# Performance work log

Measured on AMD Instinct MI355X. Metric: run time of the kernel, lower is better.

Reference implementation:

```python
import jax, jax.numpy as jnp
import numpy as np

B, NMAX, D, H = 8, 8192, 256, 8
DH = D // H  # 32
EPS = 1e-5


def _ln(x, g, b):
    mu = jnp.mean(x, axis=-1, keepdims=True)
    var = jnp.mean((x - mu) ** 2, axis=-1, keepdims=True)
    return (x - mu) / jnp.sqrt(var + EPS) * g + b


def setup_inputs() -> dict:
    key = jax.random.key(0)
    ks = jax.random.split(key, 14)
    s = 1.0 / np.sqrt(D)

    def lin(k):
        kw, kb = jax.random.split(k)
        W = jax.random.uniform(kw, (D, D), minval=-s, maxval=s, dtype=jnp.float32)
        b = jax.random.uniform(kb, (D,), minval=-s, maxval=s, dtype=jnp.float32)
        return W, b

    Wh, bh = lin(ks[0])
    Wq, bq = lin(ks[1])
    Wk, bk = lin(ks[2])
    Wv, bv = lin(ks[3])
    Wout, bout = lin(ks[4])
    return {
        "x": jax.random.normal(ks[5], (B * NMAX, D), dtype=jnp.float32),
        "node_prob": jax.random.uniform(ks[6], (B, NMAX), dtype=jnp.float32),
        "Wh": Wh, "bh": bh,
        "Wq": Wq, "bq": bq,
        "Wk": Wk, "bk": bk,
        "Wv": Wv, "bv": bv,
        "Wout": Wout, "bout": bout,
        "ln1_g": jnp.ones((D,), jnp.float32), "ln1_b": jnp.zeros((D,), jnp.float32),
        "ln2_g": jnp.ones((D,), jnp.float32), "ln2_b": jnp.zeros((D,), jnp.float32),
        "beta_b": jnp.full((D,), 0.5, jnp.float32),  # self.b with beta=0.5 >= 0
    }


def reference(x, node_prob, Wh, bh, Wq, bq, Wk, bk, Wv, bv, Wout, bout,
              ln1_g, ln1_b, ln2_g, ln2_b, beta_b):
    x0 = _ln(x, ln1_g, ln1_b)          # [N, D] input_norm
    h = x0 @ Wh + bh                   # [N, D]
    xd = x0.reshape(B, NMAX, D)        # to_dense_batch (equal-size graphs)
    k = jax.nn.sigmoid(xd @ Wk + bk)   # [B, Nmax, D]
    q = jax.nn.sigmoid(xd @ Wq + bq)   # qk_shared=False
    v = xd @ Wv + bv
    k = k * node_prob[:, :, None]      # node-prob weighting
    q = q.reshape(B, NMAX, H, DH)
    k = k.reshape(B, NMAX, H, DH)
    v = v.reshape(B, NMAX, H, DH)
    kv = jnp.einsum('bnhd,bnhe->bhde', k, v)        # k^T v per head
    num = jnp.einsum('bnhd,bhde->bnhe', q, kv)      # q . kv
    den = jnp.einsum('bnhd,bhd->bnh', q, jnp.sum(k, axis=1))[..., None]
    att = (num / den).reshape(B * NMAX, D)
    out = _ln(att, ln2_g, ln2_b) * (h + beta_b)     # norm(x) * (h + beta)
    out = jax.nn.relu(out @ Wout + bout)            # dropout p=0 / eval: identity
    return out + x0                                  # residual=True
```

## Files before the change

kernel.cpp:

```cpp
#include <hip/hip_runtime.h>
#include <cstdint>


#define DEVI __device__ __forceinline__

typedef __attribute__((ext_vector_type(8))) short bf16x8;
typedef __attribute__((ext_vector_type(4))) float f32x4;

DEVI ushort f2bf(float f) {
  uint32_t u = __float_as_uint(f);
  u += 0x7FFFu + ((u >> 16) & 1u);
  return (ushort)(u >> 16);
}
DEVI float bf2f(ushort h) { return __uint_as_float(((uint32_t)h) << 16); }

DEVI void gload_lds16(const void* g, void* l) {
  __builtin_amdgcn_global_load_lds((const __attribute__((address_space(1))) void*)g,
                                   (__attribute__((address_space(3))) void*)l, 16, 0, 0);
}
DEVI void vm_drain() { asm volatile("s_waitcnt vmcnt(0)" ::: "memory"); }

__global__ __launch_bounds__(256)
void prep_k(const float* __restrict__ Wh, const float* __restrict__ Wq,
            const float* __restrict__ Wk, const float* __restrict__ Wv,
            const float* __restrict__ Wout,
            const float* __restrict__ bh, const float* __restrict__ bq,
            const float* __restrict__ bk, const float* __restrict__ bv,
            ushort* __restrict__ Wcat_t, ushort* __restrict__ Woutt,
            float* __restrict__ bcat, float* __restrict__ kv, float* __restrict__ ksum)
{
  int idx = blockIdx.x * 256 + threadIdx.x;
  if (idx < 262144) {
    int j = idx >> 8, kk = idx & 255;
    int g = j >> 8, jj = j & 255;
    const float* W = (g == 0) ? Wh : (g == 1) ? Wq : (g == 2) ? Wk : Wv;
    Wcat_t[idx] = f2bf(W[kk * 256 + jj]);
  }
  int i2 = idx - 262144;
  if (i2 >= 0 && i2 < 65536) {
    int j = i2 >> 8, kk = i2 & 255;
    Woutt[i2] = f2bf(Wout[kk * 256 + j]);
  }
  int i3 = idx - (262144 + 65536);
  if (i3 >= 0 && i3 < 1024) {
    int g = i3 >> 8, jj = i3 & 255;
    const float* bb = (g == 0) ? bh : (g == 1) ? bq : (g == 2) ? bk : bv;
    bcat[i3] = bb[jj];
  }
  int i4 = idx - (262144 + 65536 + 1024);
  if (i4 >= 0 && i4 < 65536) kv[i4] = 0.0f;
  int i5 = idx - (262144 + 65536 + 1024 + 65536);
  if (i5 >= 0 && i5 < 2048) ksum[i5] = 0.0f;
}

__global__ __launch_bounds__(256)
void ln1_k(const float* __restrict__ x, const float* __restrict__ g1,
           const float* __restrict__ b1, ushort* __restrict__ x0b)
{
  const int t = threadIdx.x, l = t & 63, w = t >> 6;
  const size_t r = (size_t)blockIdx.x * 4 + w;
  const float4 xv = *(const float4*)&x[r * 256 + l * 4];
  float s = xv.x + xv.y + xv.z + xv.w;
  float sq = xv.x * xv.x + xv.y * xv.y + xv.z * xv.z + xv.w * xv.w;
#pragma unroll
  for (int off = 1; off < 64; off <<= 1) { s += __shfl_xor(s, off); sq += __shfl_xor(sq, off); }
  const float mean = s * (1.0f / 256.0f);
  const float var = sq * (1.0f / 256.0f) - mean * mean;
  const float rstd = rsqrtf(var + 1e-5f);
  const float4 g4 = *(const float4*)&g1[l * 4];
  const float4 b4 = *(const float4*)&b1[l * 4];
  ushort4 o;
  o.x = f2bf((xv.x - mean) * rstd * g4.x + b4.x);
  o.y = f2bf((xv.y - mean) * rstd * g4.y + b4.y);
  o.z = f2bf((xv.z - mean) * rstd * g4.z + b4.z);
  o.w = f2bf((xv.w - mean) * rstd * g4.w + b4.w);
  *(ushort4*)&x0b[r * 256 + l * 4] = o;
}

template <int MODE>
__global__ __launch_bounds__(256, 4)
void gemm_bf16_k(const ushort* __restrict__ A, const ushort* __restrict__ Bt,
                 const float* __restrict__ bias, const float* __restrict__ node_prob,
                 const ushort* __restrict__ x0b, ushort* __restrict__ outb,
                 float* __restrict__ outf)
{
  __shared__ ushort smem[16384];
  const int t = threadIdx.x;
  const int l = t & 63;
  const int w = t >> 6;
  const int wr = w >> 1, wc = w & 1;
  const int nNB = (MODE == 0) ? 8 : 2;
  const int per = gridDim.x >> 3;
  const int tile = (blockIdx.x & 7) * per + (blockIdx.x >> 3);
  const int m0 = (tile / nNB) * 128, n0 = (tile % nNB) * 128;
  const int sr = t >> 2;
  const int sd = t & 3;
  const int ssl = sd ^ ((t >> 3) & 3);
  f32x4 acc[4][4] = {};

  auto stage = [&](int buf, int kt) {
#pragma unroll
    for (int i = 0; i < 2; ++i) {
      int row = i * 64 + sr;
      gload_lds16(&A[(size_t)(m0 + row) * 256 + kt * 32 + ssl * 8],
                  &smem[buf * 4096 + row * 32 + sd * 8]);
    }
#pragma unroll
    for (int i = 0; i < 2; ++i) {
      int row = i * 64 + sr;
      gload_lds16(&Bt[(size_t)(n0 + row) * 256 + kt * 32 + ssl * 8],
                  &smem[8192 + buf * 4096 + row * 32 + sd * 8]);
    }
  };

  stage(0, 0);
  vm_drain();
  __syncthreads();
  const int fr = l & 15;
  const int fq = l >> 4;
  const int fsl = (fq ^ ((l >> 1) & 3)) * 8;
#pragma unroll
  for (int kt = 0; kt < 8; ++kt) {
    const int cur = kt & 1;
    if (kt < 7) stage(cur ^ 1, kt + 1);
    bf16x8 af[4], bfr[4];
#pragma unroll
    for (int f = 0; f < 4; ++f) {
      af[f]  = *(const bf16x8*)&smem[cur * 4096 + (wr * 64 + f * 16 + fr) * 32 + fsl];
      bfr[f] = *(const bf16x8*)&smem[8192 + cur * 4096 + (wc * 64 + f * 16 + fr) * 32 + fsl];
    }
#pragma unroll
    for (int fm = 0; fm < 4; ++fm)
#pragma unroll
      for (int fn = 0; fn < 4; ++fn)
        acc[fm][fn] = __builtin_amdgcn_mfma_f32_16x16x32_bf16(af[fm], bfr[fn], acc[fm][fn], 0, 0, 0);
    vm_drain();
    __syncthreads();
  }

  float biasv[4];
#pragma unroll
  for (int fn = 0; fn < 4; ++fn) biasv[fn] = bias[n0 + wc * 64 + fn * 16 + fr];
  const int g = n0 >> 8;
#pragma unroll
  for (int fm = 0; fm < 4; ++fm) {
#pragma unroll
    for (int fn = 0; fn < 4; ++fn) {
#pragma unroll
      for (int i = 0; i < 4; ++i) {
        const int row = wr * 64 + fm * 16 + fq * 4 + i;
        const int col = wc * 64 + fn * 16 + fr;
        float v = acc[fm][fn][i] + biasv[fn];
        if (MODE == 0) {
          if (g == 1 || g == 2) v = 1.0f / (1.0f + __expf(-v));
          if (g == 2) v *= node_prob[m0 + row];
        } else {
          v = fmaxf(v, 0.0f);
        }
        smem[row * 128 + (col ^ ((row & 7) << 4))] = f2bf(v);
      }
    }
  }
  __syncthreads();
#pragma unroll
  for (int it = 0; it < 8; ++it) {
    const int row = w * 32 + it * 4 + fq;
    const int c8 = fr * 8;
    bf16x8 u = *(const bf16x8*)&smem[row * 128 + (c8 ^ ((row & 7) << 4))];
    if (MODE == 0) {
      *(bf16x8*)&outb[(size_t)(m0 + row) * 1024 + n0 + c8] = u;
    } else {
      bf16x8 xv = *(const bf16x8*)&x0b[(size_t)(m0 + row) * 256 + n0 + c8];
      float4 o0, o1;
      o0.x = bf2f((ushort)u[0]) + bf2f((ushort)xv[0]);
      o0.y = bf2f((ushort)u[1]) + bf2f((ushort)xv[1]);
      o0.z = bf2f((ushort)u[2]) + bf2f((ushort)xv[2]);
      o0.w = bf2f((ushort)u[3]) + bf2f((ushort)xv[3]);
      o1.x = bf2f((ushort)u[4]) + bf2f((ushort)xv[4]);
      o1.y = bf2f((ushort)u[5]) + bf2f((ushort)xv[5]);
      o1.z = bf2f((ushort)u[6]) + bf2f((ushort)xv[6]);
      o1.w = bf2f((ushort)u[7]) + bf2f((ushort)xv[7]);
      *(float4*)&outf[(size_t)(m0 + row) * 256 + n0 + c8] = o0;
      *(float4*)&outf[(size_t)(m0 + row) * 256 + n0 + c8 + 4] = o1;
    }
  }
}

__global__ __launch_bounds__(256)
void kvred_k(const ushort* __restrict__ hqkv, float* __restrict__ kv, float* __restrict__ ksum)
{
  __shared__ ushort kt[64 * 32];
  __shared__ ushort vt[64 * 32];
  const int bh = blockIdx.x >> 5, chunk = blockIdx.x & 31;
  const int b = bh >> 3, h = bh & 7;
  const int t = threadIdx.x;
  const int d = t >> 3, e0 = (t & 7) * 4;
  const int lrow = t >> 2, lseg = t & 3;
  float a0 = 0, a1 = 0, a2 = 0, a3 = 0, ks = 0;
  const size_t base = (size_t)b * 8192 + chunk * 256;
  for (int sub = 0; sub < 4; ++sub) {
    size_t grow = (base + sub * 64 + lrow) * 1024;
    gload_lds16(&hqkv[grow + 512 + h * 32 + lseg * 8], &kt[lrow * 32 + lseg * 8]);
    gload_lds16(&hqkv[grow + 768 + h * 32 + lseg * 8], &vt[lrow * 32 + lseg * 8]);
    vm_drain();
    __syncthreads();
#pragma unroll 8
    for (int nn = 0; nn < 64; ++nn) {
      float kd = bf2f(kt[nn * 32 + d]);
      ushort4 vv = *(const ushort4*)&vt[nn * 32 + e0];
      a0 += kd * bf2f(vv.x);
      a1 += kd * bf2f(vv.y);
      a2 += kd * bf2f(vv.z);
      a3 += kd * bf2f(vv.w);
      ks += kd;
    }
    __syncthreads();
  }
  float* kvp = &kv[(size_t)bh * 1024 + d * 32 + e0];
  atomicAdd(kvp + 0, a0);
  atomicAdd(kvp + 1, a1);
  atomicAdd(kvp + 2, a2);
  atomicAdd(kvp + 3, a3);
  if ((t & 7) == 0) atomicAdd(&ksum[bh * 32 + d], ks);
}

__global__ __launch_bounds__(256)
void attnz_k(const ushort* __restrict__ hqkv, const float* __restrict__ kv,
             const float* __restrict__ ksum, const float* __restrict__ g2,
             const float* __restrict__ b2, const float* __restrict__ beta,
             ushort* __restrict__ zb)
{
  __shared__ float kv_s[8192];
  __shared__ float ks_s[256];
  __shared__ float q_s[16][256];
  const int t = threadIdx.x, l = t & 63, w = t >> 6;
  const int r0 = blockIdx.x * 16;
  const int b = r0 >> 13;
#pragma unroll
  for (int i = 0; i < 8; ++i)
    *(float4*)&kv_s[i * 1024 + t * 4] = *(const float4*)&kv[(size_t)b * 8192 + i * 1024 + t * 4];
  if (t < 64) *(float4*)&ks_s[t * 4] = *(const float4*)&ksum[b * 256 + t * 4];
#pragma unroll
  for (int rr = 0; rr < 4; ++rr) {
    int r = r0 + w * 4 + rr;
    ushort4 qv = *(const ushort4*)&hqkv[(size_t)r * 1024 + 256 + l * 4];
    float4 qf = {bf2f(qv.x), bf2f(qv.y), bf2f(qv.z), bf2f(qv.w)};
    *(float4*)&q_s[w * 4 + rr][l * 4] = qf;
  }
  __syncthreads();

  const int h = l >> 3, e0 = (l & 7) * 4;
  float num[4][4] = {};
  float den[4] = {0.0f, 0.0f, 0.0f, 0.0f};
#pragma unroll
  for (int dl = 0; dl < 8; ++dl) {
    const float4 ks4 = *(const float4*)&ks_s[h * 32 + dl * 4];
    float4 kvv[4];
#pragma unroll
    for (int c = 0; c < 4; ++c)
      kvv[c] = *(const float4*)&kv_s[h * 1024 + (dl * 4 + c) * 32 + e0];
#pragma unroll
    for (int rr = 0; rr < 4; ++rr) {
      const float4 q4 = *(const float4*)&q_s[w * 4 + rr][h * 32 + dl * 4];
      den[rr] += q4.x * ks4.x + q4.y * ks4.y + q4.z * ks4.z + q4.w * ks4.w;
      num[rr][0] += q4.x * kvv[0].x + q4.y * kvv[1].x + q4.z * kvv[2].x + q4.w * kvv[3].x;
      num[rr][1] += q4.x * kvv[0].y + q4.y * kvv[1].y + q4.z * kvv[2].y + q4.w * kvv[3].y;
      num[rr][2] += q4.x * kvv[0].z + q4.y * kvv[1].z + q4.z * kvv[2].z + q4.w * kvv[3].z;
      num[rr][3] += q4.x * kvv[0].w + q4.y * kvv[1].w + q4.z * kvv[2].w + q4.w * kvv[3].w;
    }
  }
  const float4 g4 = *(const float4*)&g2[l * 4];
  const float4 bb4 = *(const float4*)&b2[l * 4];
  const float4 be4 = *(const float4*)&beta[l * 4];
#pragma unroll
  for (int rr = 0; rr < 4; ++rr) {
    const int r = r0 + w * 4 + rr;
    const float inv = 1.0f / den[rr];
    float a0 = num[rr][0] * inv, a1 = num[rr][1] * inv;
    float a2 = num[rr][2] * inv, a3 = num[rr][3] * inv;
    float s = a0 + a1 + a2 + a3;
    float sq = a0 * a0 + a1 * a1 + a2 * a2 + a3 * a3;
#pragma unroll
    for (int off = 1; off < 64; off <<= 1) { s += __shfl_xor(s, off); sq += __shfl_xor(sq, off); }
    const float mean = s * (1.0f / 256.0f);
    const float var = sq * (1.0f / 256.0f) - mean * mean;
    const float rstd = rsqrtf(var + 1e-5f);
    ushort4 hv = *(const ushort4*)&hqkv[(size_t)r * 1024 + l * 4];
    ushort4 o;
    o.x = f2bf(((a0 - mean) * rstd * g4.x + bb4.x) * (bf2f(hv.x) + be4.x));
    o.y = f2bf(((a1 - mean) * rstd * g4.y + bb4.y) * (bf2f(hv.y) + be4.y));
    o.z = f2bf(((a2 - mean) * rstd * g4.z + bb4.z) * (bf2f(hv.z) + be4.z));
    o.w = f2bf(((a3 - mean) * rstd * g4.w + bb4.w) * (bf2f(hv.w) + be4.w));
    *(ushort4*)&zb[(size_t)r * 256 + l * 4] = o;
  }
}

extern "C" void kernel_launch(void* const* d_in, const int* in_sizes, int n_in,
                              void* d_out, int out_size, void* d_ws, size_t ws_size,
                              hipStream_t stream)
{
  const float* x    = (const float*)d_in[0];
  const float* np_  = (const float*)d_in[1];
  const float* Wh   = (const float*)d_in[2];
  const float* bh   = (const float*)d_in[3];
  const float* Wq   = (const float*)d_in[4];
  const float* bq   = (const float*)d_in[5];
  const float* Wk   = (const float*)d_in[6];
  const float* bk   = (const float*)d_in[7];
  const float* Wv   = (const float*)d_in[8];
  const float* bv   = (const float*)d_in[9];
  const float* Wout = (const float*)d_in[10];
  const float* bout = (const float*)d_in[11];
  const float* ln1g = (const float*)d_in[12];
  const float* ln1b = (const float*)d_in[13];
  const float* ln2g = (const float*)d_in[14];
  const float* ln2b = (const float*)d_in[15];
  const float* beta = (const float*)d_in[16];
  float* out = (float*)d_out;

  uintptr_t p = (uintptr_t)d_ws;
  ushort* x0b    = (ushort*)p; p += (size_t)65536 * 256 * 2;
  ushort* hqkv   = (ushort*)p; p += (size_t)65536 * 1024 * 2;
  ushort* zb     = (ushort*)p; p += (size_t)65536 * 256 * 2;
  ushort* Wcat_t = (ushort*)p; p += (size_t)1024 * 256 * 2;
  ushort* Woutt  = (ushort*)p; p += (size_t)256 * 256 * 2;
  float*  bcat   = (float*)p;  p += (size_t)1024 * 4;
  float*  kv     = (float*)p;  p += (size_t)65536 * 4;
  float*  ksum   = (float*)p;  p += (size_t)2048 * 4;

  prep_k<<<1548, 256, 0, stream>>>(Wh, Wq, Wk, Wv, Wout, bh, bq, bk, bv,
                                   Wcat_t, Woutt, bcat, kv, ksum);
  ln1_k<<<16384, 256, 0, stream>>>(x, ln1g, ln1b, x0b);
  gemm_bf16_k<0><<<4096, 256, 0, stream>>>(x0b, Wcat_t, bcat, np_, nullptr, hqkv, nullptr);
  kvred_k<<<2048, 256, 0, stream>>>(hqkv, kv, ksum);
  attnz_k<<<4096, 256, 0, stream>>>(hqkv, kv, ksum, ln2g, ln2b, beta, zb);
  gemm_bf16_k<1><<<1024, 256, 0, stream>>>(zb, Woutt, bout, nullptr, x0b, nullptr, out);
}
```

Baseline: 215.5 us.

## Load GEMM fragments directly from global memory into registers, bypassing LDS

Removes the LDS double-buffered staging in the bf16 GEMM. Each wave now loads its A and B MFMA fragments straight from global memory into registers, processing K in two halves, with B held in registers per half. The launch bound drops from 4 to 2 blocks per CU to make room for the larger register footprint. This drops LDS traffic and block-level barriers, but it gives up sharing of tiles between waves, so global and L2 reads are duplicated, and occupancy may fall.

```diff
diff --git a/kernel.cpp b/kernel.cpp
--- a/kernel.cpp
+++ b/kernel.cpp
@@ -78,7 +78,7 @@
 }
 
 template <int MODE>
-__global__ __launch_bounds__(256, 4)
+__global__ __launch_bounds__(256, 2)
 void gemm_bf16_k(const ushort* __restrict__ A, const ushort* __restrict__ Bt,
                  const float* __restrict__ bias, const float* __restrict__ node_prob,
                  const ushort* __restrict__ x0b, ushort* __restrict__ outb,
@@ -93,49 +93,33 @@
   const int per = gridDim.x >> 3;
   const int tile = (blockIdx.x & 7) * per + (blockIdx.x >> 3);
   const int m0 = (tile / nNB) * 128, n0 = (tile % nNB) * 128;
-  const int sr = t >> 2;
-  const int sd = t & 3;
-  const int ssl = sd ^ ((t >> 3) & 3);
-  f32x4 acc[4][4] = {};
-
-  auto stage = [&](int buf, int kt) {
-#pragma unroll
-    for (int i = 0; i < 2; ++i) {
-      int row = i * 64 + sr;
-      gload_lds16(&A[(size_t)(m0 + row) * 256 + kt * 32 + ssl * 8],
-                  &smem[buf * 4096 + row * 32 + sd * 8]);
-    }
-#pragma unroll
-    for (int i = 0; i < 2; ++i) {
-      int row = i * 64 + sr;
-      gload_lds16(&Bt[(size_t)(n0 + row) * 256 + kt * 32 + ssl * 8],
-                  &smem[8192 + buf * 4096 + row * 32 + sd * 8]);
-    }
-  };
-
-  stage(0, 0);
-  vm_drain();
-  __syncthreads();
   const int fr = l & 15;
   const int fq = l >> 4;
-  const int fsl = (fq ^ ((l >> 1) & 3)) * 8;
-#pragma unroll
-  for (int kt = 0; kt < 8; ++kt) {
-    const int cur = kt & 1;
-    if (kt < 7) stage(cur ^ 1, kt + 1);
-    bf16x8 af[4], bfr[4];
-#pragma unroll
-    for (int f = 0; f < 4; ++f) {
-      af[f]  = *(const bf16x8*)&smem[cur * 4096 + (wr * 64 + f * 16 + fr) * 32 + fsl];
-      bfr[f] = *(const bf16x8*)&smem[8192 + cur * 4096 + (wc * 64 + f * 16 + fr) * 32 + fsl];
-    }
-#pragma unroll
-    for (int fm = 0; fm < 4; ++fm)
-#pragma unroll
-      for (int fn = 0; fn < 4; ++fn)
-        acc[fm][fn] = __builtin_amdgcn_mfma_f32_16x16x32_bf16(af[fm], bfr[fn], acc[fm][fn], 0, 0, 0);
-    vm_drain();
-    __syncthreads();
+
+  const ushort* arow = &A[(size_t)(m0 + wr * 64 + fr) * 256 + fq * 8];
+  const ushort* brow = &Bt[(size_t)(n0 + wc * 64 + fr) * 256 + fq * 8];
+  f32x4 acc[4][4] = {};
+
+#pragma unroll
+  for (int h = 0; h < 2; ++h) {
+    bf16x8 breg[4][4];
+#pragma unroll
+    for (int fn = 0; fn < 4; ++fn)
+#pragma unroll
+      for (int q = 0; q < 4; ++q)
+        breg[fn][q] = *(const bf16x8*)&brow[(size_t)fn * 16 * 256 + h * 128 + q * 32];
+#pragma unroll
+    for (int q = 0; q < 4; ++q) {
+      bf16x8 af[4];
+#pragma unroll
+      for (int fm = 0; fm < 4; ++fm)
+        af[fm] = *(const bf16x8*)&arow[(size_t)fm * 16 * 256 + h * 128 + q * 32];
+#pragma unroll
+      for (int fm = 0; fm < 4; ++fm)
+#pragma unroll
+        for (int fn = 0; fn < 4; ++fn)
+          acc[fm][fn] = __builtin_amdgcn_mfma_f32_16x16x32_bf16(af[fm], breg[fn][q], acc[fm][fn], 0, 0, 0);
+    }
   }
 
   float biasv[4];
```

New measurement: 319.2 us. +48.2%, slower.
